# Kernel optimization log

Hardware: AMD Instinct MI355X
Metric: run time of the kernel (lower is better)

The kernel has to match this reference:

```python
import jax, jax.numpy as jnp
import numpy as np

B, H, S, D = 2, 8, 2048, 64
WINDOW = 3            # local_attention_window (default in torch forward)
FRAC = 0.3            # percentage_frac hardcoded in create_window_tensor call
MASK_FILL = -1.0e9


def window_kernel(window, frac):
    # create_window_tensor: [ (1-f)^n ... (1-f)^1, 1, (1-f)^1 ... (1-f)^n ]
    n = (window - 1) // 2
    side = np.array([(1.0 - frac) ** i for i in range(n, 0, -1)], dtype=np.float32)
    vals = np.concatenate([side, np.array([1.0], np.float32), side[::-1]])
    return jnp.asarray(vals)


def setup_inputs() -> dict:
    key = jax.random.key(0)
    kq, kk, kv = jax.random.split(key, 3)
    queries = jax.random.normal(kq, (B, H, S, D), jnp.float32)
    keys = jax.random.normal(kk, (B, H, S, D), jnp.float32)
    values = jax.random.normal(kv, (B, H, S, D), jnp.float32)
    # causal mask: True positions are filled with -1e9 (masked_fill semantics)
    mask = jnp.triu(jnp.ones((S, S), dtype=bool), 1)[None, None]  # [1,1,S,S]
    # linear_bias: nn.Parameter(torch.zeros(Sk)) created inside forward
    beta = jnp.zeros((S,), jnp.float32)
    return {"queries": queries, "keys": keys, "values": values,
            "beta": beta, "mask": mask}


def reference(queries, keys, values, beta, mask):
    d = keys.shape[-1]
    # scores = Q K^T / sqrt(d)
    scores = jnp.einsum("bhqd,bhkd->bhqk", queries, keys) / jnp.sqrt(
        jnp.asarray(d, queries.dtype))
    scores = jnp.where(mask, jnp.asarray(MASK_FILL, scores.dtype), scores)
    # include_local_attention=True, local_attention_dim_vertical=False:
    # the torch code transposes, conv2d with a [1,W] kernel along the last
    # axis, transposes back -> 1D cross-correlation along the QUERY axis.
    # Kernel is symmetric so correlation == convolution. Zero padding.
    kern = window_kernel(WINDOW, FRAC)
    p = (WINDOW - 1) // 2
    xp = jnp.pad(scores, ((0, 0), (0, 0), (p, p), (0, 0)))
    Sq = scores.shape[2]
    scores = sum(kern[i] * jax.lax.dynamic_slice_in_dim(xp, i, Sq, axis=2)
                 for i in range(WINDOW))
    # linear_bias=True: add zero-initialized per-key-position bias
    scores = scores + beta  # broadcasts over last dim [Sk]
    weights = jax.nn.softmax(scores, axis=-1)
    return jnp.einsum("bhqk,bhkd->bhqd", weights, values)
```

## Files before the change

kernel.cpp:

```cpp
#include <hip/hip_runtime.h>


typedef short bf16x8 __attribute__((ext_vector_type(8)));
typedef float f32x4  __attribute__((ext_vector_type(4)));

constexpr int S_ = 2048;
constexpr int D_ = 64;
constexpr float LOG2E = 1.44269504088896341f;
constexpr float KSC = 0.125f * LOG2E;

template <bool B> struct BC { static constexpr bool v = B; };

__device__ __forceinline__ unsigned pk2(float lo, float hi) {
    union { float f; unsigned u; } a, b;
    a.f = lo; b.f = hi;
    return __builtin_amdgcn_perm(b.u + 0x8000u, a.u + 0x8000u, 0x07060302u);
}

__global__ __launch_bounds__(256)
void cvt8(const float* __restrict__ K, const float* __restrict__ V,
          unsigned short* __restrict__ F)
{
    __shared__ float T[64][68];

    const int bid = blockIdx.x;
    const int hd = bid & 15, tt = bid >> 4;
    const float* Kt = K + ((size_t)hd * S_ + tt * 64) * D_;
    const float* Vt = V + ((size_t)hd * S_ + tt * 64) * D_;
    unsigned short* Ft = F + (size_t)(hd * 32 + tt) * 8192;

    const int t = threadIdx.x;
    const int key = t >> 2, d0 = (t & 3) << 4;

    {
        const float* vp = Vt + key * D_ + d0;
        #pragma unroll
        for (int i = 0; i < 4; ++i) {
            float4 v4 = *(const float4*)(vp + 4 * i);
            T[d0 + 4 * i + 0][key] = v4.x;
            T[d0 + 4 * i + 1][key] = v4.y;
            T[d0 + 4 * i + 2][key] = v4.z;
            T[d0 + 4 * i + 3][key] = v4.w;
        }
    }

    {
        const float* kp = Kt + key * D_ + d0;
        float4 a = *(const float4*)(kp);
        float4 b = *(const float4*)(kp + 4);
        float4 c = *(const float4*)(kp + 8);
        float4 d = *(const float4*)(kp + 12);
        uint4 w0 = make_uint4(pk2(a.x, a.y), pk2(a.z, a.w), pk2(b.x, b.y), pk2(b.z, b.w));
        uint4 w1 = make_uint4(pk2(c.x, c.y), pk2(c.z, c.w), pk2(d.x, d.y), pk2(d.z, d.w));
        const int r5 = key & 31;
        const int kh = key >> 5, mb = (r5 >> 2) & 1;
        const int n = ((r5 >> 3) << 2) | (r5 & 3);
        const int hh = d0 >> 5, qd0 = (d0 >> 3) & 3;
        const int f0 = (kh << 2) | (mb << 1) | hh;
        *(uint4*)(Ft + f0 * 512 + ((qd0 << 4) | n) * 8)       = w0;
        *(uint4*)(Ft + f0 * 512 + (((qd0 + 1) << 4) | n) * 8) = w1;
    }
    __syncthreads();

    #pragma unroll
    for (int s = 0; s < 2; ++s) {
        const int slot = t + s * 256;
        const int fr = slot >> 6, lane = slot & 63;
        const int kh = fr >> 2, mb = fr & 3, n = lane & 15, qd = lane >> 4;
        const float* row = &T[mb * 16 + n][kh * 32 + qd * 8];
        uint4 w = make_uint4(pk2(row[0], row[1]), pk2(row[2], row[3]),
                             pk2(row[4], row[5]), pk2(row[6], row[7]));
        *(uint4*)(Ft + (8 + fr) * 512 + lane * 8) = w;
    }
}

__global__ __launch_bounds__(512, 4)
void attn14(const float* __restrict__ Q, const float* __restrict__ beta,
            const unsigned short* __restrict__ F, float* __restrict__ out)
{
    __shared__ float slab[2][64][72];
    __shared__ float bl[S_];

    const int bid = blockIdx.x;
    const int hd = bid & 15;
    const int rest = bid >> 4;
    const int j = (rest < 16) ? (31 - 2 * rest) : (2 * (rest - 16));

    const int q0 = j << 6;
    const int nt = j + 1;

    const float* Qh = Q + (size_t)hd * S_ * D_;
    const unsigned short* Fh = F + (size_t)hd * 32 * 8192;

    const int t = threadIdx.x, lane = t & 63;
    const int wv = t >> 6;
    const int kh = wv & 1, par = (wv >> 1) & 1, qh = wv >> 2;
    const int n_l = lane & 15, qd = lane >> 4;
    const int qbase = q0 + (qh << 5);

    #pragma unroll
    for (int i = 0; i < 4; ++i) bl[t + i * 512] = beta[t + i * 512] * LOG2E;
    __syncthreads();

    const int lo = lane * 8;
    int kfo[2][2], vfo[4];
    #pragma unroll
    for (int mb = 0; mb < 2; ++mb)
        #pragma unroll
        for (int hh = 0; hh < 2; ++hh)
            kfo[mb][hh] = ((kh << 2) | (mb << 1) | hh) * 512 + lo;
    #pragma unroll
    for (int mb = 0; mb < 4; ++mb)
        vfo[mb] = (8 + (kh << 2) + mb) * 512 + lo;

    const int kvo = (kh << 5) + (qd << 3);

    auto ld_ka = [&](int tile, bf16x8 (&ka)[2][2]) {
        const unsigned short* fp = Fh + (size_t)tile * 8192;
        ka[0][0] = *(const bf16x8*)(fp + kfo[0][0]);
        ka[0][1] = *(const bf16x8*)(fp + kfo[0][1]);
        ka[1][0] = *(const bf16x8*)(fp + kfo[1][0]);
        ka[1][1] = *(const bf16x8*)(fp + kfo[1][1]);
    };

    bf16x8 qb[2][2];
    #pragma unroll
    for (int ng = 0; ng < 2; ++ng) {
        const int q = qbase + (ng << 4) + n_l;
        const float wp = (q > 0) ? 0.7f : 0.0f;
        const float wn = (q + 1 < S_) ? 0.7f : 0.0f;
        const float* qc = Qh + (size_t)q * D_;
        const float* qpp = qc - ((q > 0) ? D_ : 0);
        const float* qnn = qc + ((q + 1 < S_) ? D_ : 0);
        #pragma unroll
        for (int hh = 0; hh < 2; ++hh) {
            const int d0 = (hh << 5) + (qd << 3);
            float4 c0 = *(const float4*)(qc + d0),  c1 = *(const float4*)(qc + d0 + 4);
            float4 p0 = *(const float4*)(qpp + d0), p1 = *(const float4*)(qpp + d0 + 4);
            float4 n0 = *(const float4*)(qnn + d0), n1 = *(const float4*)(qnn + d0 + 4);
            float e0 = fmaf(wn, n0.x, fmaf(wp, p0.x, c0.x));
            float e1 = fmaf(wn, n0.y, fmaf(wp, p0.y, c0.y));
            float e2 = fmaf(wn, n0.z, fmaf(wp, p0.z, c0.z));
            float e3 = fmaf(wn, n0.w, fmaf(wp, p0.w, c0.w));
            float e4 = fmaf(wn, n1.x, fmaf(wp, p1.x, c1.x));
            float e5 = fmaf(wn, n1.y, fmaf(wp, p1.y, c1.y));
            float e6 = fmaf(wn, n1.z, fmaf(wp, p1.z, c1.z));
            float e7 = fmaf(wn, n1.w, fmaf(wp, p1.w, c1.w));
            union { unsigned u[4]; bf16x8 v; } qu;
            qu.u[0] = pk2(e0, e1); qu.u[1] = pk2(e2, e3);
            qu.u[2] = pk2(e4, e5); qu.u[3] = pk2(e6, e7);
            qb[ng][hh] = qu.v;
        }
    }

    f32x4 o[4][2];
    float l[2] = {0.0f, 0.0f};
    #pragma unroll
    for (int mb = 0; mb < 4; ++mb)
        #pragma unroll
        for (int ng = 0; ng < 2; ++ng) o[mb][ng] = (f32x4){0, 0, 0, 0};

    auto comp = [&](int tile, bf16x8 (&kaC)[2][2], bf16x8 (&kaN)[2][2], auto prc) {
        constexpr bool PRE = decltype(prc)::v;
        const int kb = (tile << 6) + kvo;
        const unsigned short* fp = Fh + (size_t)tile * 8192;
        bf16x8 vb[4];
        #pragma unroll
        for (int mb = 0; mb < 4; ++mb)
            vb[mb] = *(const bf16x8*)(fp + vfo[mb]);
        float4 b0 = *(const float4*)&bl[kb];
        float4 b1 = *(const float4*)&bl[kb + 4];
        const float bt[8] = {b0.x, b0.y, b0.z, b0.w, b1.x, b1.y, b1.z, b1.w};
        const f32x4 zz = {0, 0, 0, 0};
        f32x4 acc[2][2];
        #pragma unroll
        for (int mb = 0; mb < 2; ++mb)
            #pragma unroll
            for (int ng = 0; ng < 2; ++ng) {
                f32x4 a = __builtin_amdgcn_mfma_f32_16x16x32_bf16(kaC[mb][0], qb[ng][0], zz, 0, 0, 0);
                acc[mb][ng] = __builtin_amdgcn_mfma_f32_16x16x32_bf16(kaC[mb][1], qb[ng][1], a, 0, 0, 0);
            }
        if constexpr (PRE) ld_ka(tile + 2, kaN);
        const bool dm = (tile == nt - 1);
        #pragma unroll
        for (int ng = 0; ng < 2; ++ng) {
            const int qr = qbase + (ng << 4) + n_l;
            float pv[8];
            float la = 0.0f;
            #pragma unroll
            for (int jj = 0; jj < 8; ++jj) {
                const int mb = jj >> 2, r = jj & 3;
                float sv = fmaf(acc[mb][ng][r], KSC, bt[jj]);
                if (dm) {
                    const int key = kb + jj;
                    if (!((key < qr) || (qr == 0 && key == 0))) sv = -1.0e30f;
                }
                pv[jj] = __builtin_amdgcn_exp2f(sv);
                la += pv[jj];
            }
            l[ng] += la;
            union { unsigned u[4]; bf16x8 v; } pf;
            pf.u[0] = pk2(pv[0], pv[1]);
            pf.u[1] = pk2(pv[2], pv[3]);
            pf.u[2] = pk2(pv[4], pv[5]);
            pf.u[3] = pk2(pv[6], pv[7]);
            #pragma unroll
            for (int mb = 0; mb < 4; ++mb)
                o[mb][ng] = __builtin_amdgcn_mfma_f32_16x16x32_bf16(vb[mb], pf.v, o[mb][ng], 0, 0, 0);
        }
    };

    bf16x8 kaA[2][2], kaB[2][2];
    int it = par;
    if (it < nt) {
        ld_ka(it, kaA);
        while (it + 4 < nt) {
            comp(it,     kaA, kaB, BC<true>{});
            comp(it + 2, kaB, kaA, BC<true>{});
            it += 4;
        }
        if (it + 2 < nt) {
            comp(it,     kaA, kaB, BC<true>{});
            comp(it + 2, kaB, kaA, BC<false>{});
        } else {
            comp(it, kaA, kaB, BC<false>{});
        }
    }

    #pragma unroll
    for (int ng = 0; ng < 2; ++ng) {
        l[ng] += __shfl_xor(l[ng], 16);
        l[ng] += __shfl_xor(l[ng], 32);
    }
    if (par == 1) {
        #pragma unroll
        for (int ng = 0; ng < 2; ++ng) {
            const int row = (qh << 5) + (ng << 4) + n_l;
            #pragma unroll
            for (int mb = 0; mb < 4; ++mb)
                *(float4*)&slab[kh][row][(mb << 4) + (qd << 2)] =
                    make_float4(o[mb][ng][0], o[mb][ng][1], o[mb][ng][2], o[mb][ng][3]);
            if (qd == 0) slab[kh][row][64] = l[ng];
        }
    }
    __syncthreads();
    if (par == 0) {
        #pragma unroll
        for (int ng = 0; ng < 2; ++ng) {
            const int row = (qh << 5) + (ng << 4) + n_l;
            #pragma unroll
            for (int mb = 0; mb < 4; ++mb) {
                float4 pv4 = *(float4*)&slab[kh][row][(mb << 4) + (qd << 2)];
                o[mb][ng][0] += pv4.x; o[mb][ng][1] += pv4.y;
                o[mb][ng][2] += pv4.z; o[mb][ng][3] += pv4.w;
            }
            l[ng] += slab[kh][row][64];
            if (kh == 0) {
                #pragma unroll
                for (int mb = 0; mb < 4; ++mb)
                    *(float4*)&slab[0][row][(mb << 4) + (qd << 2)] =
                        make_float4(o[mb][ng][0], o[mb][ng][1], o[mb][ng][2], o[mb][ng][3]);
                if (qd == 0) slab[0][row][64] = l[ng];
            }
        }
    }
    __syncthreads();
    if (par == 0 && kh == 1) {
        #pragma unroll
        for (int ng = 0; ng < 2; ++ng) {
            const int row = (qh << 5) + (ng << 4) + n_l;
            const float inv = 1.0f / (l[ng] + slab[0][row][64]);
            float* op = out + ((size_t)hd * S_ + q0 + row) * D_ + (qd << 2);
            #pragma unroll
            for (int mb = 0; mb < 4; ++mb) {
                float4 pv4 = *(float4*)&slab[0][row][(mb << 4) + (qd << 2)];
                *(float4*)(op + (mb << 4)) =
                    make_float4((o[mb][ng][0] + pv4.x) * inv, (o[mb][ng][1] + pv4.y) * inv,
                                (o[mb][ng][2] + pv4.z) * inv, (o[mb][ng][3] + pv4.w) * inv);
            }
        }
    }
}

extern "C" void kernel_launch(void* const* d_in, const int* in_sizes, int n_in,
                              void* d_out, int out_size, void* d_ws, size_t ws_size,
                              hipStream_t stream) {
    const float* Q    = (const float*)d_in[0];
    const float* K    = (const float*)d_in[1];
    const float* V    = (const float*)d_in[2];
    const float* beta = (const float*)d_in[3];
    float* out = (float*)d_out;

    unsigned short* F = (unsigned short*)d_ws;

    cvt8<<<dim3(512), 256, 0, stream>>>(K, V, F);
    attn14<<<dim3(512), 512, 0, stream>>>(Q, beta, F, out);
}
```

Measured before the change: 133.1 us.

## Stage K/V tiles through double-buffered LDS and split waves by query rows

The attention kernel now loads each 64-key bf16 K/V tile cooperatively into a double-buffered shared-memory buffer, prefetching the next tile into registers while computing the current one. Before this, each wave read its fragments straight from global memory and waves were split by key-tile parity. Waves are now split across 16-row query groups instead, which removes the parity reduction and leaves a simpler two-way kh merge. The intent is to cut redundant global/L2 fragment traffic. In exchange it adds a block-wide barrier on every tile, and the launch bound drops to 2 blocks per CU, which may reduce latency hiding.

```diff
diff --git a/kernel.cpp b/kernel.cpp
--- a/kernel.cpp
+++ b/kernel.cpp
@@ -8,8 +8,6 @@
 constexpr int D_ = 64;
 constexpr float LOG2E = 1.44269504088896341f;
 constexpr float KSC = 0.125f * LOG2E;
-
-template <bool B> struct BC { static constexpr bool v = B; };
 
 __device__ __forceinline__ unsigned pk2(float lo, float hi) {
     union { float f; unsigned u; } a, b;
@@ -74,11 +72,12 @@
     }
 }
 
-__global__ __launch_bounds__(512, 4)
-void attn14(const float* __restrict__ Q, const float* __restrict__ beta,
+__global__ __launch_bounds__(512, 2)
+void attn19(const float* __restrict__ Q, const float* __restrict__ beta,
             const unsigned short* __restrict__ F, float* __restrict__ out)
 {
-    __shared__ float slab[2][64][72];
+    __shared__ __align__(16) unsigned short fbuf[2][8192];
+    __shared__ float slab[64][68];
     __shared__ float bl[S_];
 
     const int bid = blockIdx.x;
@@ -94,13 +93,12 @@
 
     const int t = threadIdx.x, lane = t & 63;
     const int wv = t >> 6;
-    const int kh = wv & 1, par = (wv >> 1) & 1, qh = wv >> 2;
+    const int kh = wv & 1, qh = wv >> 1;
     const int n_l = lane & 15, qd = lane >> 4;
-    const int qbase = q0 + (qh << 5);
+    const int qbase = q0 + (qh << 4);
 
     #pragma unroll
     for (int i = 0; i < 4; ++i) bl[t + i * 512] = beta[t + i * 512] * LOG2E;
-    __syncthreads();
 
     const int lo = lane * 8;
     int kfo[2][2], vfo[4];
@@ -115,18 +113,9 @@
 
     const int kvo = (kh << 5) + (qd << 3);
 
-    auto ld_ka = [&](int tile, bf16x8 (&ka)[2][2]) {
-        const unsigned short* fp = Fh + (size_t)tile * 8192;
-        ka[0][0] = *(const bf16x8*)(fp + kfo[0][0]);
-        ka[0][1] = *(const bf16x8*)(fp + kfo[0][1]);
-        ka[1][0] = *(const bf16x8*)(fp + kfo[1][0]);
-        ka[1][1] = *(const bf16x8*)(fp + kfo[1][1]);
-    };
-
-    bf16x8 qb[2][2];
-    #pragma unroll
-    for (int ng = 0; ng < 2; ++ng) {
-        const int q = qbase + (ng << 4) + n_l;
+    bf16x8 qb[2];
+    {
+        const int q = qbase + n_l;
         const float wp = (q > 0) ? 0.7f : 0.0f;
         const float wn = (q + 1 < S_) ? 0.7f : 0.0f;
         const float* qc = Qh + (size_t)q * D_;
@@ -149,48 +138,55 @@
             union { unsigned u[4]; bf16x8 v; } qu;
             qu.u[0] = pk2(e0, e1); qu.u[1] = pk2(e2, e3);
             qu.u[2] = pk2(e4, e5); qu.u[3] = pk2(e6, e7);
-            qb[ng][hh] = qu.v;
-        }
-    }
-
-    f32x4 o[4][2];
-    float l[2] = {0.0f, 0.0f};
-    #pragma unroll
-    for (int mb = 0; mb < 4; ++mb)
-        #pragma unroll
-        for (int ng = 0; ng < 2; ++ng) o[mb][ng] = (f32x4){0, 0, 0, 0};
-
-    auto comp = [&](int tile, bf16x8 (&kaC)[2][2], bf16x8 (&kaN)[2][2], auto prc) {
-        constexpr bool PRE = decltype(prc)::v;
-        const int kb = (tile << 6) + kvo;
-        const unsigned short* fp = Fh + (size_t)tile * 8192;
-        bf16x8 vb[4];
-        #pragma unroll
-        for (int mb = 0; mb < 4; ++mb)
-            vb[mb] = *(const bf16x8*)(fp + vfo[mb]);
-        float4 b0 = *(const float4*)&bl[kb];
-        float4 b1 = *(const float4*)&bl[kb + 4];
-        const float bt[8] = {b0.x, b0.y, b0.z, b0.w, b1.x, b1.y, b1.z, b1.w};
-        const f32x4 zz = {0, 0, 0, 0};
-        f32x4 acc[2][2];
-        #pragma unroll
-        for (int mb = 0; mb < 2; ++mb)
-            #pragma unroll
-            for (int ng = 0; ng < 2; ++ng) {
-                f32x4 a = __builtin_amdgcn_mfma_f32_16x16x32_bf16(kaC[mb][0], qb[ng][0], zz, 0, 0, 0);
-                acc[mb][ng] = __builtin_amdgcn_mfma_f32_16x16x32_bf16(kaC[mb][1], qb[ng][1], a, 0, 0, 0);
-            }
-        if constexpr (PRE) ld_ka(tile + 2, kaN);
-        const bool dm = (tile == nt - 1);
-        #pragma unroll
-        for (int ng = 0; ng < 2; ++ng) {
-            const int qr = qbase + (ng << 4) + n_l;
+            qb[hh] = qu.v;
+        }
+    }
+
+    f32x4 o[4];
+    float l = 0.0f;
+    #pragma unroll
+    for (int mb = 0; mb < 4; ++mb) o[mb] = (f32x4){0, 0, 0, 0};
+
+    uint4 sA, sB;
+    {
+        const unsigned short* gs = Fh + t * 16;
+        sA = *(const uint4*)gs;
+        sB = *(const uint4*)(gs + 8);
+        unsigned short* db = &fbuf[0][t * 16];
+        *(uint4*)db = sA;
+        *(uint4*)(db + 8) = sB;
+    }
+    __syncthreads();
+
+    for (int tt = 0; tt < nt; ++tt) {
+        if (tt + 1 < nt) {
+            const unsigned short* gs = Fh + (size_t)(tt + 1) * 8192 + t * 16;
+            sA = *(const uint4*)gs;
+            sB = *(const uint4*)(gs + 8);
+        }
+        {
+            const unsigned short* fb = fbuf[tt & 1];
+            bf16x8 ka00 = *(const bf16x8*)(fb + kfo[0][0]);
+            bf16x8 ka01 = *(const bf16x8*)(fb + kfo[0][1]);
+            bf16x8 ka10 = *(const bf16x8*)(fb + kfo[1][0]);
+            bf16x8 ka11 = *(const bf16x8*)(fb + kfo[1][1]);
+            const int kb = (tt << 6) + kvo;
+            const float4 b0 = *(const float4*)&bl[kb];
+            const float4 b1 = *(const float4*)&bl[kb + 4];
+            const float bt[8] = {b0.x, b0.y, b0.z, b0.w, b1.x, b1.y, b1.z, b1.w};
+            const f32x4 zz = {0, 0, 0, 0};
+            f32x4 acc[2];
+            acc[0] = __builtin_amdgcn_mfma_f32_16x16x32_bf16(ka01, qb[1],
+                     __builtin_amdgcn_mfma_f32_16x16x32_bf16(ka00, qb[0], zz, 0, 0, 0), 0, 0, 0);
+            acc[1] = __builtin_amdgcn_mfma_f32_16x16x32_bf16(ka11, qb[1],
+                     __builtin_amdgcn_mfma_f32_16x16x32_bf16(ka10, qb[0], zz, 0, 0, 0), 0, 0, 0);
+            const bool dm = (tt == nt - 1);
+            const int qr = qbase + n_l;
             float pv[8];
             float la = 0.0f;
             #pragma unroll
             for (int jj = 0; jj < 8; ++jj) {
-                const int mb = jj >> 2, r = jj & 3;
-                float sv = fmaf(acc[mb][ng][r], KSC, bt[jj]);
+                float sv = fmaf(acc[jj >> 2][jj & 3], KSC, bt[jj]);
                 if (dm) {
                     const int key = kb + jj;
                     if (!((key < qr) || (qr == 0 && key == 0))) sv = -1.0e30f;
@@ -198,86 +194,49 @@
                 pv[jj] = __builtin_amdgcn_exp2f(sv);
                 la += pv[jj];
             }
-            l[ng] += la;
+            l += la;
             union { unsigned u[4]; bf16x8 v; } pf;
             pf.u[0] = pk2(pv[0], pv[1]);
             pf.u[1] = pk2(pv[2], pv[3]);
             pf.u[2] = pk2(pv[4], pv[5]);
             pf.u[3] = pk2(pv[6], pv[7]);
-            #pragma unroll
-            for (int mb = 0; mb < 4; ++mb)
-                o[mb][ng] = __builtin_amdgcn_mfma_f32_16x16x32_bf16(vb[mb], pf.v, o[mb][ng], 0, 0, 0);
-        }
-    };
-
-    bf16x8 kaA[2][2], kaB[2][2];
-    int it = par;
-    if (it < nt) {
-        ld_ka(it, kaA);
-        while (it + 4 < nt) {
-            comp(it,     kaA, kaB, BC<true>{});
-            comp(it + 2, kaB, kaA, BC<true>{});
-            it += 4;
-        }
-        if (it + 2 < nt) {
-            comp(it,     kaA, kaB, BC<true>{});
-            comp(it + 2, kaB, kaA, BC<false>{});
-        } else {
-            comp(it, kaA, kaB, BC<false>{});
-        }
-    }
-
-    #pragma unroll
-    for (int ng = 0; ng < 2; ++ng) {
-        l[ng] += __shfl_xor(l[ng], 16);
-        l[ng] += __shfl_xor(l[ng], 32);
-    }
-    if (par == 1) {
-        #pragma unroll
-        for (int ng = 0; ng < 2; ++ng) {
-            const int row = (qh << 5) + (ng << 4) + n_l;
-            #pragma unroll
-            for (int mb = 0; mb < 4; ++mb)
-                *(float4*)&slab[kh][row][(mb << 4) + (qd << 2)] =
-                    make_float4(o[mb][ng][0], o[mb][ng][1], o[mb][ng][2], o[mb][ng][3]);
-            if (qd == 0) slab[kh][row][64] = l[ng];
-        }
+            bf16x8 vb0 = *(const bf16x8*)(fb + vfo[0]);
+            bf16x8 vb1 = *(const bf16x8*)(fb + vfo[1]);
+            bf16x8 vb2 = *(const bf16x8*)(fb + vfo[2]);
+            bf16x8 vb3 = *(const bf16x8*)(fb + vfo[3]);
+            o[0] = __builtin_amdgcn_mfma_f32_16x16x32_bf16(vb0, pf.v, o[0], 0, 0, 0);
+            o[1] = __builtin_amdgcn_mfma_f32_16x16x32_bf16(vb1, pf.v, o[1], 0, 0, 0);
+            o[2] = __builtin_amdgcn_mfma_f32_16x16x32_bf16(vb2, pf.v, o[2], 0, 0, 0);
+            o[3] = __builtin_amdgcn_mfma_f32_16x16x32_bf16(vb3, pf.v, o[3], 0, 0, 0);
+        }
+        if (tt + 1 < nt) {
+            unsigned short* db = &fbuf[(tt + 1) & 1][t * 16];
+            *(uint4*)db = sA;
+            *(uint4*)(db + 8) = sB;
+        }
+        __syncthreads();
+    }
+
+    l += __shfl_xor(l, 16);
+    l += __shfl_xor(l, 32);
+    const int row = (qh << 4) + n_l;
+    if (kh == 1) {
+        #pragma unroll
+        for (int mb = 0; mb < 4; ++mb)
+            *(float4*)&slab[row][(mb << 4) + (qd << 2)] =
+                make_float4(o[mb][0], o[mb][1], o[mb][2], o[mb][3]);
+        if (qd == 0) slab[row][64] = l;
     }
     __syncthreads();
-    if (par == 0) {
-        #pragma unroll
-        for (int ng = 0; ng < 2; ++ng) {
-            const int row = (qh << 5) + (ng << 4) + n_l;
-            #pragma unroll
-            for (int mb = 0; mb < 4; ++mb) {
-                float4 pv4 = *(float4*)&slab[kh][row][(mb << 4) + (qd << 2)];
-                o[mb][ng][0] += pv4.x; o[mb][ng][1] += pv4.y;
-                o[mb][ng][2] += pv4.z; o[mb][ng][3] += pv4.w;
-            }
-            l[ng] += slab[kh][row][64];
-            if (kh == 0) {
-                #pragma unroll
-                for (int mb = 0; mb < 4; ++mb)
-                    *(float4*)&slab[0][row][(mb << 4) + (qd << 2)] =
-                        make_float4(o[mb][ng][0], o[mb][ng][1], o[mb][ng][2], o[mb][ng][3]);
-                if (qd == 0) slab[0][row][64] = l[ng];
-            }
-        }
-    }
-    __syncthreads();
-    if (par == 0 && kh == 1) {
-        #pragma unroll
-        for (int ng = 0; ng < 2; ++ng) {
-            const int row = (qh << 5) + (ng << 4) + n_l;
-            const float inv = 1.0f / (l[ng] + slab[0][row][64]);
-            float* op = out + ((size_t)hd * S_ + q0 + row) * D_ + (qd << 2);
-            #pragma unroll
-            for (int mb = 0; mb < 4; ++mb) {
-                float4 pv4 = *(float4*)&slab[0][row][(mb << 4) + (qd << 2)];
-                *(float4*)(op + (mb << 4)) =
-                    make_float4((o[mb][ng][0] + pv4.x) * inv, (o[mb][ng][1] + pv4.y) * inv,
-                                (o[mb][ng][2] + pv4.z) * inv, (o[mb][ng][3] + pv4.w) * inv);
-            }
+    if (kh == 0) {
+        const float inv = 1.0f / (l + slab[row][64]);
+        float* op = out + ((size_t)hd * S_ + q0 + row) * D_ + (qd << 2);
+        #pragma unroll
+        for (int mb = 0; mb < 4; ++mb) {
+            float4 pv4 = *(float4*)&slab[row][(mb << 4) + (qd << 2)];
+            *(float4*)(op + (mb << 4)) =
+                make_float4((o[mb][0] + pv4.x) * inv, (o[mb][1] + pv4.y) * inv,
+                            (o[mb][2] + pv4.z) * inv, (o[mb][3] + pv4.w) * inv);
         }
     }
 }
@@ -294,5 +253,5 @@
     unsigned short* F = (unsigned short*)d_ws;
 
     cvt8<<<dim3(512), 256, 0, stream>>>(K, V, F);
-    attn14<<<dim3(512), 512, 0, stream>>>(Q, beta, F, out);
-}
+    attn19<<<dim3(512), 512, 0, stream>>>(Q, beta, F, out);
+}
```

Measured after the change: 108.0 us. 18.8% less time.
